# Kernel tuning notes

Hardware: AMD Instinct MI355X
Metric: run time of the kernel (lower is better)

## Reference

```python
import jax, jax.numpy as jnp
import numpy as np

D_MODEL = 2048
N_HEADS = 16
D_HEAD = D_MODEL // N_HEADS
EPS = 1e-5


def _layernorm(x, g, b):
    m = jnp.mean(x, axis=-1, keepdims=True)
    v = jnp.mean(jnp.square(x - m), axis=-1, keepdims=True)
    return (x - m) * jax.lax.rsqrt(v + EPS) * g + b


def _mha(x, Wq, bq, Wk, bk, Wv, bv, Wo, bo):
    b, s, _ = x.shape
    # torch Linear: y = x @ W.T + b ; W is [out, in]
    q = (x @ Wq.T + bq).reshape(b, s, N_HEADS, D_HEAD).transpose(0, 2, 1, 3)
    k = (x @ Wk.T + bk).reshape(b, s, N_HEADS, D_HEAD).transpose(0, 2, 1, 3)
    v = (x @ Wv.T + bv).reshape(b, s, N_HEADS, D_HEAD).transpose(0, 2, 1, 3)
    scores = jnp.einsum('bhqd,bhkd->bhqk', q, k) / np.sqrt(D_HEAD).astype(np.float32)
    score = jax.nn.softmax(scores, axis=-1)
    o = jnp.einsum('bhqk,bhkd->bhqd', score, v)
    # NOTE: original does .contiguous().view(b, -1, d_model) WITHOUT transposing
    # heads back -> head-major flattening. Replicated faithfully via reshape.
    o = o.reshape(b, s, D_MODEL)
    return o @ Wo.T + bo, score


def setup_inputs() -> dict:
    key = jax.random.key(0)
    ks = jax.random.split(key, 16)
    sd = 1.0 / np.sqrt(D_MODEL)
    sdf = 1.0 / np.sqrt(4 * D_MODEL)
    d = {
        'x': jax.random.normal(ks[0], (2, 2048, D_MODEL), jnp.float32),
        'Wq': jax.random.uniform(ks[1], (D_MODEL, D_MODEL), jnp.float32, -sd, sd),
        'bq': jnp.zeros((D_MODEL,), jnp.float32),
        'Wk': jax.random.uniform(ks[2], (D_MODEL, D_MODEL), jnp.float32, -sd, sd),
        'bk': jnp.zeros((D_MODEL,), jnp.float32),
        'Wv': jax.random.uniform(ks[3], (D_MODEL, D_MODEL), jnp.float32, -sd, sd),
        'bv': jnp.zeros((D_MODEL,), jnp.float32),
        'Wo': jax.random.uniform(ks[4], (D_MODEL, D_MODEL), jnp.float32, -sd, sd),
        'bo': jnp.zeros((D_MODEL,), jnp.float32),
        'ln1_g': jnp.ones((D_MODEL,), jnp.float32),
        'ln1_b': jnp.zeros((D_MODEL,), jnp.float32),
        'W1': jax.random.uniform(ks[5], (4 * D_MODEL, D_MODEL), jnp.float32, -sd, sd),
        'b1': jnp.zeros((4 * D_MODEL,), jnp.float32),
        'W2': jax.random.uniform(ks[6], (D_MODEL, 4 * D_MODEL), jnp.float32, -sdf, sdf),
        'b2': jnp.zeros((D_MODEL,), jnp.float32),
        'ln2_g': jnp.ones((D_MODEL,), jnp.float32),
        'ln2_b': jnp.zeros((D_MODEL,), jnp.float32),
    }
    return d


def reference(x, Wq, bq, Wk, bk, Wv, bv, Wo, bo, ln1_g, ln1_b, W1, b1, W2, b2, ln2_g, ln2_b):
    # Pre-norm self-attention block (is_post_norm=False, is_cross=False).
    # Dropout is identity (eval mode).
    x_ = _layernorm(x, ln1_g, ln1_b)
    attn_out, score = _mha(x_, Wq, bq, Wk, bk, Wv, bv, Wo, bo)
    x = x + attn_out
    x_ = _layernorm(x, ln2_g, ln2_b)
    h = jax.nn.relu(x_ @ W1.T + b1)
    x = x + (h @ W2.T + b2)
    return x, score
```

## Files before the change

kernel.cpp:

```cpp
#include <hip/hip_runtime.h>
#include <math.h>

#define D_MODEL 2048
#define NHEADS  16
#define DHEAD   128
#define SEQ     2048
#define BATCH   2
#define ROWS    (BATCH * SEQ)
#define D_FF    (4 * D_MODEL)

typedef __attribute__((ext_vector_type(8))) short bf16x8;
typedef __attribute__((ext_vector_type(4))) float f32x4;

__device__ __forceinline__ unsigned short f2bf(float f) {
    unsigned int u = __float_as_uint(f);
    u += 0x7fffu + ((u >> 16) & 1u);
    return (unsigned short)(u >> 16);
}

__device__ __forceinline__ float block_reduce(float v, int is_max) {
    __shared__ float tmp[4];
    #pragma unroll
    for (int o = 32; o > 0; o >>= 1) {
        float other = __shfl_down(v, o, 64);
        v = is_max ? fmaxf(v, other) : (v + other);
    }
    __syncthreads();
    if ((threadIdx.x & 63) == 0) tmp[threadIdx.x >> 6] = v;
    __syncthreads();
    float r = is_max ? fmaxf(fmaxf(tmp[0], tmp[1]), fmaxf(tmp[2], tmp[3]))
                     : (tmp[0] + tmp[1] + tmp[2] + tmp[3]);
    return r;
}

__global__ __launch_bounds__(256)
void castbf_kernel(const float* __restrict__ in, unsigned short* __restrict__ out, int n4)
{
    int i = blockIdx.x * 256 + threadIdx.x;
    if (i < n4) {
        float4 v = ((const float4*)in)[i];
        ushort4 o;
        o.x = f2bf(v.x); o.y = f2bf(v.y); o.z = f2bf(v.z); o.w = f2bf(v.w);
        ((ushort4*)out)[i] = o;
    }
}

__global__ __launch_bounds__(256)
void ln_kernel(const float* __restrict__ x, const float* __restrict__ g,
               const float* __restrict__ b, unsigned short* __restrict__ y)
{
    __shared__ float row[D_MODEL];
    const long r = blockIdx.x;
    const float4* xr = (const float4*)(x + r * D_MODEL);
    float s = 0.f;
    for (int i = threadIdx.x; i < D_MODEL / 4; i += 256) {
        float4 v = xr[i];
        ((float4*)row)[i] = v;
        s += v.x + v.y + v.z + v.w;
    }
    s = block_reduce(s, 0);
    const float mean = s * (1.f / D_MODEL);
    float vs = 0.f;
    for (int i = threadIdx.x; i < D_MODEL / 4; i += 256) {
        float4 v = ((const float4*)row)[i];
        float dx = v.x - mean; vs += dx * dx;
        dx = v.y - mean; vs += dx * dx;
        dx = v.z - mean; vs += dx * dx;
        dx = v.w - mean; vs += dx * dx;
    }
    vs = block_reduce(vs, 0);
    const float inv = rsqrtf(vs * (1.f / D_MODEL) + 1e-5f);
    const float4* g4 = (const float4*)g;
    const float4* b4 = (const float4*)b;
    for (int i = threadIdx.x; i < D_MODEL / 4; i += 256) {
        float4 v = ((const float4*)row)[i];
        float4 gg = g4[i], bb = b4[i];
        ushort4 o;
        o.x = f2bf((v.x - mean) * inv * gg.x + bb.x);
        o.y = f2bf((v.y - mean) * inv * gg.y + bb.y);
        o.z = f2bf((v.z - mean) * inv * gg.z + bb.z);
        o.w = f2bf((v.w - mean) * inv * gg.w + bb.w);
        *(ushort4*)(y + r * D_MODEL + i * 4) = o;
    }
}

__global__ __launch_bounds__(256)
void softmax_kernel(float* __restrict__ sc, unsigned short* __restrict__ pb)
{
    __shared__ float row[SEQ];
    float* p = sc + (long)blockIdx.x * SEQ;
    unsigned short* pbf = pb + (long)blockIdx.x * SEQ;
    float m = -1e30f;
    for (int i = threadIdx.x; i < SEQ / 4; i += 256) {
        float4 v = ((const float4*)p)[i];
        ((float4*)row)[i] = v;
        m = fmaxf(m, fmaxf(fmaxf(v.x, v.y), fmaxf(v.z, v.w)));
    }
    m = block_reduce(m, 1);
    float sum = 0.f;
    for (int i = threadIdx.x; i < SEQ; i += 256) {
        float e = expf(row[i] - m);
        row[i] = e;
        sum += e;
    }
    sum = block_reduce(sum, 0);
    const float inv = 1.f / sum;
    for (int i = threadIdx.x; i < SEQ / 4; i += 256) {
        float4 v = ((const float4*)row)[i];
        v.x *= inv; v.y *= inv; v.z *= inv; v.w *= inv;
        ((float4*)p)[i] = v;
        ushort4 o;
        o.x = f2bf(v.x); o.y = f2bf(v.y); o.z = f2bf(v.z); o.w = f2bf(v.w);
        ((ushort4*)pbf)[i] = o;
    }
}

constexpr int BK = 64;

__device__ __forceinline__ void stage_lds(const unsigned short* gbase, int ld,
                                          unsigned short* lds, int wid, int lane)
{
    const int l8 = lane >> 3, c8 = lane & 7;
    #pragma unroll
    for (int i = 0; i < 4; ++i) {
        const int rowb = wid * 32 + i * 8;
        const unsigned short* src = gbase + (size_t)(rowb + l8) * ld + c8 * 8;
        unsigned short* dst = lds + rowb * 64;
        __builtin_amdgcn_global_load_lds(
            (const __attribute__((address_space(1))) unsigned int*)src,
            (__attribute__((address_space(3))) unsigned int*)dst, 16, 0, 0);
    }
}

template<bool OUTBF>
__global__ __launch_bounds__(256)
void gemm_mfma(const unsigned short* __restrict__ A, int lda,
               const unsigned short* __restrict__ B, int ldb,
               const float* __restrict__ bias, int biasM,
               const float* __restrict__ resid,
               void* __restrict__ Cv, int ldc,
               int Kdim, float scale, int relu,
               long sAb, long sAh, long sBb, long sBh, long sCb, long sCh,
               int nh)
{
    __shared__ __align__(16) char smem[32768];
    unsigned short* As = (unsigned short*)smem;
    unsigned short* Bs = As + 128 * BK;

    const int z  = blockIdx.z;
    const int zb = z / nh, zh = z % nh;
    A += zb * sAb + zh * sAh;
    B += zb * sBb + zh * sBh;
    const long coff = zb * sCb + zh * sCh;
    float*          Cf = (float*)Cv + coff;
    unsigned short* Ch = (unsigned short*)Cv + coff;

    const int bm = blockIdx.y * 128;
    const int bn = blockIdx.x * 128;
    const int t  = threadIdx.x;
    const int lane = t & 63;
    const int wid  = t >> 6;
    const int wr = wid >> 1, wc = wid & 1;
    const int li = lane & 15;
    const int g  = lane >> 4;

    f32x4 acc[4][4];
    #pragma unroll
    for (int i = 0; i < 4; ++i)
        #pragma unroll
        for (int j = 0; j < 4; ++j) acc[i][j] = (f32x4){0.f, 0.f, 0.f, 0.f};

    int aoffs[4], boffs[4];
    #pragma unroll
    for (int m = 0; m < 4; ++m) {
        const int ra = wr * 64 + m * 16 + li;
        const int rb = wc * 64 + m * 16 + li;
        aoffs[m] = ra * 128 + (g << 4);
        boffs[m] = rb * 128 + (g << 4);
    }

    for (int k0 = 0; k0 < Kdim; k0 += BK) {
        stage_lds(A + (size_t)bm * lda + k0, lda, As, wid, lane);
        stage_lds(B + (size_t)bn * ldb + k0, ldb, Bs, wid, lane);
        __syncthreads();
        #pragma unroll
        for (int kk = 0; kk < 2; ++kk) {
            const int kb = kk * 64;
            bf16x8 a[4], b[4];
            #pragma unroll
            for (int m = 0; m < 4; ++m) {
                a[m] = *(const bf16x8*)((const char*)As + (aoffs[m] ^ kb));
                b[m] = *(const bf16x8*)((const char*)Bs + (boffs[m] ^ kb));
            }
            #pragma unroll
            for (int m = 0; m < 4; ++m)
                #pragma unroll
                for (int n = 0; n < 4; ++n)
                    acc[m][n] = __builtin_amdgcn_mfma_f32_16x16x32_bf16(
                                    a[m], b[n], acc[m][n], 0, 0, 0);
        }
        __syncthreads();
    }

    float* epi = (float*)smem;
    const int g4 = g * 4;
    const int lrow_r = t >> 2, q = t & 3;
    #pragma unroll
    for (int p = 0; p < 2; ++p) {
        __syncthreads();
        #pragma unroll
        for (int mm = 0; mm < 2; ++mm) {
            const int m = 2 * p + mm;
            #pragma unroll
            for (int n = 0; n < 4; ++n) {
                const int col = wc * 64 + n * 16 + li;
                #pragma unroll
                for (int r = 0; r < 4; ++r) {
                    const int lrow = wr * 32 + mm * 16 + g4 + r;
                    const int byteoff = lrow * 512 + ((((col >> 2) ^ (lrow & 7)) << 4)) + (col & 3) * 4;
                    *(float*)((char*)epi + byteoff) = acc[m][n][r];
                }
            }
        }
        __syncthreads();
        const long grow = bm + (lrow_r >> 5) * 64 + p * 32 + (lrow_r & 31);
        const int col0 = bn + q * 32;
        float v[32];
        #pragma unroll
        for (int i = 0; i < 8; ++i) {
            const int byteoff = lrow_r * 512 + ((((q * 8 + i) ^ (lrow_r & 7)) << 4));
            *(f32x4*)&v[i * 4] = *(const f32x4*)((const char*)epi + byteoff);
        }
        #pragma unroll
        for (int i = 0; i < 32; ++i) v[i] *= scale;
        if (bias) {
            if (biasM) {
                const float bm_ = bias[grow];
                #pragma unroll
                for (int i = 0; i < 32; ++i) v[i] += bm_;
            } else {
                #pragma unroll
                for (int i = 0; i < 8; ++i) {
                    f32x4 bb = *(const f32x4*)(bias + col0 + i * 4);
                    v[i * 4 + 0] += bb[0]; v[i * 4 + 1] += bb[1];
                    v[i * 4 + 2] += bb[2]; v[i * 4 + 3] += bb[3];
                }
            }
        }
        if (resid) {
            const float* rr = resid + grow * (long)ldc + col0;
            #pragma unroll
            for (int i = 0; i < 8; ++i) {
                f32x4 r4 = *(const f32x4*)(rr + i * 4);
                v[i * 4 + 0] += r4[0]; v[i * 4 + 1] += r4[1];
                v[i * 4 + 2] += r4[2]; v[i * 4 + 3] += r4[3];
            }
        }
        if (relu) {
            #pragma unroll
            for (int i = 0; i < 32; ++i) v[i] = fmaxf(v[i], 0.f);
        }
        if (OUTBF) {
            unsigned short* cp = Ch + grow * (long)ldc + col0;
            #pragma unroll
            for (int i = 0; i < 4; ++i) {
                bf16x8 o;
                #pragma unroll
                for (int j = 0; j < 8; ++j) o[j] = (short)f2bf(v[i * 8 + j]);
                *(bf16x8*)(cp + i * 8) = o;
            }
        } else {
            float* cp = Cf + grow * (long)ldc + col0;
            #pragma unroll
            for (int i = 0; i < 8; ++i)
                *(f32x4*)(cp + i * 4) = *(const f32x4*)&v[i * 4];
        }
    }
}

extern "C" void kernel_launch(void* const* d_in, const int* in_sizes, int n_in,
                              void* d_out, int out_size, void* d_ws, size_t ws_size,
                              hipStream_t stream)
{
    const float* x    = (const float*)d_in[0];
    const float* Wq   = (const float*)d_in[1];
    const float* bq   = (const float*)d_in[2];
    const float* Wk   = (const float*)d_in[3];
    const float* bk   = (const float*)d_in[4];
    const float* Wv   = (const float*)d_in[5];
    const float* bv   = (const float*)d_in[6];
    const float* Wo   = (const float*)d_in[7];
    const float* bo   = (const float*)d_in[8];
    const float* ln1g = (const float*)d_in[9];
    const float* ln1b = (const float*)d_in[10];
    const float* W1   = (const float*)d_in[11];
    const float* b1   = (const float*)d_in[12];
    const float* W2   = (const float*)d_in[13];
    const float* b2   = (const float*)d_in[14];
    const float* ln2g = (const float*)d_in[15];
    const float* ln2b = (const float*)d_in[16];

    const long XN = (long)ROWS * D_MODEL;
    float* out_x     = (float*)d_out;
    float* out_score = out_x + XN;

    char* w = (char*)d_ws;
    unsigned short* Qb   = (unsigned short*)(w);
    unsigned short* Kb   = (unsigned short*)(w + (16u << 20));
    unsigned short* Vtb  = (unsigned short*)(w + (32u << 20));
    unsigned short* xlnb = (unsigned short*)(w + (48u << 20));
    unsigned short* hb   = (unsigned short*)(w + (64u << 20));
    float*          x1   = (float*)         (w + (128u << 20));
    unsigned short* Wqb  = (unsigned short*)(w + (160u << 20));
    unsigned short* Wkb  = (unsigned short*)(w + (168u << 20));
    unsigned short* Wvb  = (unsigned short*)(w + (176u << 20));
    unsigned short* Wob  = (unsigned short*)(w + (184u << 20));
    unsigned short* W1b  = (unsigned short*)(w + (192u << 20));
    unsigned short* W2b  = (unsigned short*)(w + (224u << 20));
    unsigned short* Pb   = (unsigned short*)(w + (256u << 20));
    unsigned short* Ohb   = xlnb;
    unsigned short* xln2b = Kb;

    const dim3 blk(256);
    const float one = 1.f;
    const float qk_scale = 0.08838834764831843f;
    const long Z4M = (long)SEQ * D_MODEL;
    const long ZSC = (long)SEQ * SEQ;
    const long ZOH = (long)SEQ * DHEAD;

    const int nW = D_MODEL * D_MODEL / 4, nF = D_FF * D_MODEL / 4;
    hipLaunchKernelGGL(castbf_kernel, dim3(nW / 256), blk, 0, stream, Wq, Wqb, nW);
    hipLaunchKernelGGL(castbf_kernel, dim3(nW / 256), blk, 0, stream, Wk, Wkb, nW);
    hipLaunchKernelGGL(castbf_kernel, dim3(nW / 256), blk, 0, stream, Wv, Wvb, nW);
    hipLaunchKernelGGL(castbf_kernel, dim3(nW / 256), blk, 0, stream, Wo, Wob, nW);
    hipLaunchKernelGGL(castbf_kernel, dim3(nF / 256), blk, 0, stream, W1, W1b, nF);
    hipLaunchKernelGGL(castbf_kernel, dim3(nF / 256), blk, 0, stream, W2, W2b, nF);

    hipLaunchKernelGGL(ln_kernel, dim3(ROWS), blk, 0, stream, x, ln1g, ln1b, xlnb);

    hipLaunchKernelGGL((gemm_mfma<true>), dim3(D_MODEL / 128, ROWS / 128, 1), blk, 0, stream,
                       xlnb, D_MODEL, Wqb, D_MODEL, bq, 0, nullptr, Qb, D_MODEL,
                       D_MODEL, one, 0, 0L, 0L, 0L, 0L, 0L, 0L, 1);
    hipLaunchKernelGGL((gemm_mfma<true>), dim3(D_MODEL / 128, ROWS / 128, 1), blk, 0, stream,
                       xlnb, D_MODEL, Wkb, D_MODEL, bk, 0, nullptr, Kb, D_MODEL,
                       D_MODEL, one, 0, 0L, 0L, 0L, 0L, 0L, 0L, 1);
    hipLaunchKernelGGL((gemm_mfma<true>), dim3(SEQ / 128, D_MODEL / 128, BATCH), blk, 0, stream,
                       Wvb, D_MODEL, xlnb, D_MODEL, bv, 1, nullptr, Vtb, SEQ,
                       D_MODEL, one, 0, 0L, 0L, Z4M, 0L, Z4M, 0L, 1);

    hipLaunchKernelGGL((gemm_mfma<false>), dim3(SEQ / 128, SEQ / 128, BATCH * NHEADS), blk, 0, stream,
                       Qb, D_MODEL, Kb, D_MODEL, nullptr, 0, nullptr, out_score, SEQ,
                       DHEAD, qk_scale, 0,
                       Z4M, (long)DHEAD, Z4M, (long)DHEAD, (long)NHEADS * ZSC, ZSC, NHEADS);

    hipLaunchKernelGGL(softmax_kernel, dim3(BATCH * NHEADS * SEQ), blk, 0, stream, out_score, Pb);

    hipLaunchKernelGGL((gemm_mfma<true>), dim3(DHEAD / 128, SEQ / 128, BATCH * NHEADS), blk, 0, stream,
                       Pb, SEQ, Vtb, SEQ, nullptr, 0, nullptr, Ohb, DHEAD,
                       SEQ, one, 0,
                       (long)NHEADS * ZSC, ZSC, Z4M, (long)DHEAD * SEQ,
                       (long)NHEADS * ZOH, ZOH, NHEADS);

    hipLaunchKernelGGL((gemm_mfma<false>), dim3(D_MODEL / 128, ROWS / 128, 1), blk, 0, stream,
                       Ohb, D_MODEL, Wob, D_MODEL, bo, 0, x, x1, D_MODEL,
                       D_MODEL, one, 0, 0L, 0L, 0L, 0L, 0L, 0L, 1);

    hipLaunchKernelGGL(ln_kernel, dim3(ROWS), blk, 0, stream, x1, ln2g, ln2b, xln2b);

    hipLaunchKernelGGL((gemm_mfma<true>), dim3(D_FF / 128, ROWS / 128, 1), blk, 0, stream,
                       xln2b, D_MODEL, W1b, D_MODEL, b1, 0, nullptr, hb, D_FF,
                       D_MODEL, one, 1, 0L, 0L, 0L, 0L, 0L, 0L, 1);

    hipLaunchKernelGGL((gemm_mfma<false>), dim3(D_MODEL / 128, ROWS / 128, 1), blk, 0, stream,
                       hb, D_FF, W2b, D_FF, b2, 0, x1, out_x, D_MODEL,
                       D_FF, one, 0, 0L, 0L, 0L, 0L, 0L, 0L, 1);
}
```

Before: 1.969 ms.

## Double-buffer LDS tiles in MFMA GEMM to overlap global loads with compute

Adds a DBUF template path that keeps two 32 KB LDS stages. It issues global_load_lds for the next K tile before computing the current one, which hides load latency and drops one barrier per iteration. Dynamic shared memory is used, so the launches now pass 32 KB or 64 KB. The double-buffered path is enabled for the QKV, PV, Wo and W2 GEMMs; the QK^T and W1 GEMMs keep the single-buffer path. Doubling LDS per block may reduce occupancy on the selected kernels.

```diff
diff --git a/kernel.cpp b/kernel.cpp
--- a/kernel.cpp
+++ b/kernel.cpp
@@ -132,7 +132,7 @@
     }
 }
 
-template<bool OUTBF>
+template<bool OUTBF, bool DBUF>
 __global__ __launch_bounds__(256)
 void gemm_mfma(const unsigned short* __restrict__ A, int lda,
                const unsigned short* __restrict__ B, int ldb,
@@ -143,9 +143,7 @@
                long sAb, long sAh, long sBb, long sBh, long sCb, long sCh,
                int nh)
 {
-    __shared__ __align__(16) char smem[32768];
-    unsigned short* As = (unsigned short*)smem;
-    unsigned short* Bs = As + 128 * BK;
+    extern __shared__ char smem[];
 
     const int z  = blockIdx.z;
     const int zb = z / nh, zh = z % nh;
@@ -179,18 +177,15 @@
         boffs[m] = rb * 128 + (g << 4);
     }
 
-    for (int k0 = 0; k0 < Kdim; k0 += BK) {
-        stage_lds(A + (size_t)bm * lda + k0, lda, As, wid, lane);
-        stage_lds(B + (size_t)bn * ldb + k0, ldb, Bs, wid, lane);
-        __syncthreads();
+    auto compute_tile = [&](const char* AsB, const char* BsB) {
         #pragma unroll
         for (int kk = 0; kk < 2; ++kk) {
             const int kb = kk * 64;
             bf16x8 a[4], b[4];
             #pragma unroll
             for (int m = 0; m < 4; ++m) {
-                a[m] = *(const bf16x8*)((const char*)As + (aoffs[m] ^ kb));
-                b[m] = *(const bf16x8*)((const char*)Bs + (boffs[m] ^ kb));
+                a[m] = *(const bf16x8*)(AsB + (aoffs[m] ^ kb));
+                b[m] = *(const bf16x8*)(BsB + (boffs[m] ^ kb));
             }
             #pragma unroll
             for (int m = 0; m < 4; ++m)
@@ -199,7 +194,40 @@
                     acc[m][n] = __builtin_amdgcn_mfma_f32_16x16x32_bf16(
                                     a[m], b[n], acc[m][n], 0, 0, 0);
         }
-        __syncthreads();
+    };
+
+    const unsigned short* Abase = A + (size_t)bm * lda;
+    const unsigned short* Bbase = B + (size_t)bn * ldb;
+
+    if (DBUF) {
+        stage_lds(Abase, lda, (unsigned short*)smem,           wid, lane);
+        stage_lds(Bbase, ldb, (unsigned short*)(smem + 16384), wid, lane);
+        asm volatile("s_waitcnt vmcnt(0)" ::: "memory");
+        __builtin_amdgcn_s_barrier();
+        int cur = 0;
+        for (int k0 = 0; k0 < Kdim; k0 += BK) {
+            const bool more = (k0 + BK < Kdim);
+            char* nxt = smem + (cur ^ 1) * 32768;
+            if (more) {
+                stage_lds(Abase + k0 + BK, lda, (unsigned short*)nxt,           wid, lane);
+                stage_lds(Bbase + k0 + BK, ldb, (unsigned short*)(nxt + 16384), wid, lane);
+            }
+            const char* curb = smem + cur * 32768;
+            compute_tile(curb, curb + 16384);
+            if (more) {
+                asm volatile("s_waitcnt vmcnt(0)" ::: "memory");
+                __builtin_amdgcn_s_barrier();
+                cur ^= 1;
+            }
+        }
+    } else {
+        for (int k0 = 0; k0 < Kdim; k0 += BK) {
+            stage_lds(Abase + k0, lda, (unsigned short*)smem,           wid, lane);
+            stage_lds(Bbase + k0, ldb, (unsigned short*)(smem + 16384), wid, lane);
+            __syncthreads();
+            compute_tile(smem, smem + 16384);
+            __syncthreads();
+        }
     }
 
     float* epi = (float*)smem;
@@ -327,6 +355,7 @@
     const long Z4M = (long)SEQ * D_MODEL;
     const long ZSC = (long)SEQ * SEQ;
     const long ZOH = (long)SEQ * DHEAD;
+    const unsigned LDS1 = 32768, LDS2 = 65536;
 
     const int nW = D_MODEL * D_MODEL / 4, nF = D_FF * D_MODEL / 4;
     hipLaunchKernelGGL(castbf_kernel, dim3(nW / 256), blk, 0, stream, Wq, Wqb, nW);
@@ -338,40 +367,40 @@
 
     hipLaunchKernelGGL(ln_kernel, dim3(ROWS), blk, 0, stream, x, ln1g, ln1b, xlnb);
 
-    hipLaunchKernelGGL((gemm_mfma<true>), dim3(D_MODEL / 128, ROWS / 128, 1), blk, 0, stream,
+    hipLaunchKernelGGL((gemm_mfma<true, true>), dim3(D_MODEL / 128, ROWS / 128, 1), blk, LDS2, stream,
                        xlnb, D_MODEL, Wqb, D_MODEL, bq, 0, nullptr, Qb, D_MODEL,
                        D_MODEL, one, 0, 0L, 0L, 0L, 0L, 0L, 0L, 1);
-    hipLaunchKernelGGL((gemm_mfma<true>), dim3(D_MODEL / 128, ROWS / 128, 1), blk, 0, stream,
+    hipLaunchKernelGGL((gemm_mfma<true, true>), dim3(D_MODEL / 128, ROWS / 128, 1), blk, LDS2, stream,
                        xlnb, D_MODEL, Wkb, D_MODEL, bk, 0, nullptr, Kb, D_MODEL,
                        D_MODEL, one, 0, 0L, 0L, 0L, 0L, 0L, 0L, 1);
-    hipLaunchKernelGGL((gemm_mfma<true>), dim3(SEQ / 128, D_MODEL / 128, BATCH), blk, 0, stream,
+    hipLaunchKernelGGL((gemm_mfma<true, true>), dim3(SEQ / 128, D_MODEL / 128, BATCH), blk, LDS2, stream,
                        Wvb, D_MODEL, xlnb, D_MODEL, bv, 1, nullptr, Vtb, SEQ,
                        D_MODEL, one, 0, 0L, 0L, Z4M, 0L, Z4M, 0L, 1);
 
-    hipLaunchKernelGGL((gemm_mfma<false>), dim3(SEQ / 128, SEQ / 128, BATCH * NHEADS), blk, 0, stream,
+    hipLaunchKernelGGL((gemm_mfma<false, false>), dim3(SEQ / 128, SEQ / 128, BATCH * NHEADS), blk, LDS1, stream,
                        Qb, D_MODEL, Kb, D_MODEL, nullptr, 0, nullptr, out_score, SEQ,
                        DHEAD, qk_scale, 0,
                        Z4M, (long)DHEAD, Z4M, (long)DHEAD, (long)NHEADS * ZSC, ZSC, NHEADS);
 
     hipLaunchKernelGGL(softmax_kernel, dim3(BATCH * NHEADS * SEQ), blk, 0, stream, out_score, Pb);
 
-    hipLaunchKernelGGL((gemm_mfma<true>), dim3(DHEAD / 128, SEQ / 128, BATCH * NHEADS), blk, 0, stream,
+    hipLaunchKernelGGL((gemm_mfma<true, true>), dim3(DHEAD / 128, SEQ / 128, BATCH * NHEADS), blk, LDS2, stream,
                        Pb, SEQ, Vtb, SEQ, nullptr, 0, nullptr, Ohb, DHEAD,
                        SEQ, one, 0,
                        (long)NHEADS * ZSC, ZSC, Z4M, (long)DHEAD * SEQ,
                        (long)NHEADS * ZOH, ZOH, NHEADS);
 
-    hipLaunchKernelGGL((gemm_mfma<false>), dim3(D_MODEL / 128, ROWS / 128, 1), blk, 0, stream,
+    hipLaunchKernelGGL((gemm_mfma<false, true>), dim3(D_MODEL / 128, ROWS / 128, 1), blk, LDS2, stream,
                        Ohb, D_MODEL, Wob, D_MODEL, bo, 0, x, x1, D_MODEL,
                        D_MODEL, one, 0, 0L, 0L, 0L, 0L, 0L, 0L, 1);
 
     hipLaunchKernelGGL(ln_kernel, dim3(ROWS), blk, 0, stream, x1, ln2g, ln2b, xln2b);
 
-    hipLaunchKernelGGL((gemm_mfma<true>), dim3(D_FF / 128, ROWS / 128, 1), blk, 0, stream,
+    hipLaunchKernelGGL((gemm_mfma<true, false>), dim3(D_FF / 128, ROWS / 128, 1), blk, LDS1, stream,
                        xln2b, D_MODEL, W1b, D_MODEL, b1, 0, nullptr, hb, D_FF,
                        D_MODEL, one, 1, 0L, 0L, 0L, 0L, 0L, 0L, 1);
 
-    hipLaunchKernelGGL((gemm_mfma<false>), dim3(D_MODEL / 128, ROWS / 128, 1), blk, 0, stream,
+    hipLaunchKernelGGL((gemm_mfma<false, true>), dim3(D_MODEL / 128, ROWS / 128, 1), blk, LDS2, stream,
                        hb, D_FF, W2b, D_FF, b2, 0, x1, out_x, D_MODEL,
                        D_FF, one, 0, 0L, 0L, 0L, 0L, 0L, 0L, 1);
 }
```

After: 1.838 ms. 6.7% less time.
